# Optimization experiments

Measured on AMD Instinct MI355X. Metric: run time of the kernel, lower is better.

The kernel has to match this reference:

```python
import math
import jax, jax.numpy as jnp
import numpy as np

N = 100000       # nodes
K = 32           # fixed neighbor fanout
D_IN = 128
D_OUT = 128
TPERC = 0.45


def setup_inputs() -> dict:
    key = jax.random.key(0)
    k1, k2, k3 = jax.random.split(key, 3)
    x = jax.random.normal(k1, (N, D_IN), dtype=jnp.float32)
    # nn.Linear weight [out, in], no bias
    W = jax.random.normal(k2, (D_OUT, D_IN), dtype=jnp.float32) * (1.0 / math.sqrt(D_IN))
    nbrs = jax.random.randint(k3, (N, K), 0, N, dtype=jnp.int32)
    return {"x": x, "W": W, "nbrs": nbrs}


def reference(x, W, nbrs):
    # h = Linear(x): [N, D_OUT]
    h = jnp.einsum("nd,od->no", x, W)
    # gather neighbor messages: [N, K, D_OUT]
    msgs = h[nbrs]
    # per-channel sort over the neighbor axis (matches torch.sort(dim=0) per node)
    msgs = jnp.sort(msgs, axis=1)
    remove = math.floor(K * TPERC)  # static: 14
    if remove > 0:
        msgs = msgs[:, remove:K - remove]
    # trimmed mean over remaining neighbors; activation is identity (None)
    return jnp.mean(msgs, axis=1)
```

## Files before the change

kernel.cpp:

```cpp
#include <hip/hip_runtime.h>
#include <hip/hip_fp16.h>

#define NN 100000
#define KK 32
#define DD 128

typedef _Float16 v8h __attribute__((ext_vector_type(8)));
typedef _Float16 v4h __attribute__((ext_vector_type(4)));
typedef _Float16 v2h __attribute__((ext_vector_type(2)));
typedef float    v4f __attribute__((ext_vector_type(4)));

#define LDH 136

__global__ __launch_bounds__(256)
void gemm_mfma_kernel(const float* __restrict__ x, const float* __restrict__ W,
                      _Float16* __restrict__ h) {
    __shared__ _Float16 w_lds[DD * LDH];
    __shared__ _Float16 x_lds[128 * LDH];

    const int tid = threadIdx.x;
    const int block_row = blockIdx.x * 128;

    {
        const float4* ws = (const float4*)W;
        #pragma unroll
        for (int t = 0; t < 16; ++t) {
            const int fi = tid + 256 * t;
            const int r = fi >> 5, c4 = fi & 31;
            const float4 f = ws[fi];
            v4h p = { (_Float16)f.x, (_Float16)f.y, (_Float16)f.z, (_Float16)f.w };
            *(v4h*)&w_lds[r * LDH + c4 * 4] = p;
        }
    }
    {
        const float4* xs = (const float4*)x;
        #pragma unroll
        for (int t = 0; t < 16; ++t) {
            const int fi = tid + 256 * t;
            const int r = fi >> 5, c4 = fi & 31;
            const int gr = block_row + r;
            float4 f = make_float4(0.f, 0.f, 0.f, 0.f);
            if (gr < NN) f = xs[(size_t)gr * 32 + c4];
            v4h p = { (_Float16)f.x, (_Float16)f.y, (_Float16)f.z, (_Float16)f.w };
            *(v4h*)&x_lds[r * LDH + c4 * 4] = p;
        }
    }
    __syncthreads();

    const int wv   = tid >> 6;
    const int lane = tid & 63;
    const int m    = lane & 15;
    const int quad = lane >> 4;

    const v4f zero = {0.f, 0.f, 0.f, 0.f};
    v4f acc[2][8];
    #pragma unroll
    for (int nt = 0; nt < 2; ++nt)
        #pragma unroll
        for (int ot = 0; ot < 8; ++ot) acc[nt][ot] = zero;

    #pragma unroll
    for (int ks = 0; ks < 4; ++ks) {
        const int kb = ks * 32 + quad * 8;
        const v8h xf0 = *(const v8h*)&x_lds[(wv * 32 + m) * LDH + kb];
        const v8h xf1 = *(const v8h*)&x_lds[(wv * 32 + 16 + m) * LDH + kb];
        #pragma unroll
        for (int ot = 0; ot < 8; ++ot) {
            const v8h wf = *(const v8h*)&w_lds[(ot * 16 + m) * LDH + kb];
            acc[0][ot] = __builtin_amdgcn_mfma_f32_16x16x32_f16(wf, xf0, acc[0][ot], 0, 0, 0);
            acc[1][ot] = __builtin_amdgcn_mfma_f32_16x16x32_f16(wf, xf1, acc[1][ot], 0, 0, 0);
        }
    }

    #pragma unroll
    for (int nt = 0; nt < 2; ++nt) {
        const int xr = block_row + wv * 32 + nt * 16 + m;
        if (xr < NN) {
            #pragma unroll
            for (int ot = 0; ot < 8; ++ot) {
                const v4f a = acc[nt][ot];
                v4h p = { (_Float16)a.x, (_Float16)a.y, (_Float16)a.z, (_Float16)a.w };
                *(v4h*)&h[(size_t)xr * DD + ot * 16 + quad * 4] = p;
            }
        }
    }
}

#define CEA(i, l) do { const v2h lo_ = __builtin_elementwise_min(v[i], v[l]); \
                       const v2h hi_ = __builtin_elementwise_max(v[i], v[l]); \
                       v[i] = lo_; v[l] = hi_; } while (0)
#define CED(i, l) do { const v2h lo_ = __builtin_elementwise_min(v[i], v[l]); \
                       const v2h hi_ = __builtin_elementwise_max(v[i], v[l]); \
                       v[i] = hi_; v[l] = lo_; } while (0)

__global__ __launch_bounds__(256)
void trimmed_mean_kernel(const _Float16* __restrict__ h, const int* __restrict__ nbrs,
                         float* __restrict__ out) {
    __shared__ int s_nbr[4][KK];

    const int tid = threadIdx.x;
    const int row_base = blockIdx.x * 4;

    if (tid < 128)
        s_nbr[tid >> 5][tid & 31] = nbrs[(size_t)row_base * KK + tid];
    __syncthreads();

    const int c   = tid & 63;
    const int sub = tid >> 6;
    const int row = row_base + sub;

    const v2h* hb = (const v2h*)h;

    v2h v[KK];
    #pragma unroll
    for (int k = 0; k < KK; ++k) {
        const int idx = s_nbr[sub][k];
        v[k] = hb[(size_t)idx * 64 + c];
    }

    #pragma unroll
    for (int k = 2; k <= 16; k <<= 1) {
        #pragma unroll
        for (int j = k >> 1; j > 0; j >>= 1) {
            #pragma unroll
            for (int i = 0; i < KK; ++i) {
                const int l = i ^ j;
                if (l > i) {
                    if ((i & k) == 0) CEA(i, l);
                    else              CED(i, l);
                }
            }
        }
    }
    #pragma unroll
    for (int i = 0; i < 16; ++i) CEA(i, i + 16);
    #pragma unroll
    for (int i = 0; i < 8; ++i) { CEA(i, i + 8); CEA(i + 16, i + 24); }
    CEA(8, 12); CEA(9, 13); CEA(10, 14); CEA(11, 15);
    CEA(16, 20); CEA(17, 21); CEA(18, 22); CEA(19, 23);
    CEA(12, 14); CEA(13, 15); CEA(16, 18); CEA(17, 19);
    CEA(14, 15); CEA(16, 17);

    float2 o2;
    o2.x = ((float)v[14].x + (float)v[15].x + (float)v[16].x + (float)v[17].x) * 0.25f;
    o2.y = ((float)v[14].y + (float)v[15].y + (float)v[16].y + (float)v[17].y) * 0.25f;
    ((float2*)(out + (size_t)row * DD))[c] = o2;
}

extern "C" void kernel_launch(void* const* d_in, const int* in_sizes, int n_in,
                              void* d_out, int out_size, void* d_ws, size_t ws_size,
                              hipStream_t stream) {
    const float* x    = (const float*)d_in[0];
    const float* W    = (const float*)d_in[1];
    const int*   nbrs = (const int*)d_in[2];
    float*       out  = (float*)d_out;
    _Float16*    h    = (_Float16*)d_ws;

    (void)in_sizes; (void)n_in; (void)out_size; (void)ws_size;

    gemm_mfma_kernel<<<(NN + 127) / 128, 256, 0, stream>>>(x, W, h);
    trimmed_mean_kernel<<<NN / 4, 256, 0, stream>>>(h, nbrs, out);
}
```

Baseline: 230.3 us.

## Use odd-even merge sort network with 4 channels per thread in trimmed mean

Swaps the bitonic sorting network for Batcher odd-even merge sort on each 16-element half, generated at compile time. The second half is indexed in reverse so the bitonic merge can go straight to the middle elements. Each thread now loads 8 bytes (4 fp16 channels) per neighbor and handles 8 rows per block, which halves the gather instruction count and raises per-thread ILP. The cost is higher register pressure from 64 packed registers per thread, and the hand-written packed min/max inline asm may limit compiler scheduling.

```diff
diff --git a/kernel.cpp b/kernel.cpp
--- a/kernel.cpp
+++ b/kernel.cpp
@@ -86,65 +86,98 @@
     }
 }
 
-#define CEA(i, l) do { const v2h lo_ = __builtin_elementwise_min(v[i], v[l]); \
-                       const v2h hi_ = __builtin_elementwise_max(v[i], v[l]); \
-                       v[i] = lo_; v[l] = hi_; } while (0)
-#define CED(i, l) do { const v2h lo_ = __builtin_elementwise_min(v[i], v[l]); \
-                       const v2h hi_ = __builtin_elementwise_max(v[i], v[l]); \
-                       v[i] = hi_; v[l] = lo_; } while (0)
+struct CEp { signed char a, b; };
+struct Net16 { CEp ce[63]; };
+
+constexpr int oem_merge(CEp* out, int c, int lo, int n, int r) {
+    const int m = r * 2;
+    if (m < n) {
+        c = oem_merge(out, c, lo, n, m);
+        c = oem_merge(out, c, lo + r, n, m);
+        for (int i = lo + r; i + r < lo + n; i += m) {
+            out[c].a = (signed char)i; out[c].b = (signed char)(i + r); ++c;
+        }
+    } else {
+        out[c].a = (signed char)lo; out[c].b = (signed char)(lo + r); ++c;
+    }
+    return c;
+}
+constexpr int oem_sort(CEp* out, int c, int lo, int n) {
+    if (n > 1) {
+        const int m = n / 2;
+        c = oem_sort(out, c, lo, m);
+        c = oem_sort(out, c, lo + m, m);
+        c = oem_merge(out, c, lo, n, 1);
+    }
+    return c;
+}
+constexpr Net16 make_net16() {
+    Net16 net{};
+    (void)oem_sort(net.ce, 0, 0, 16);
+    return net;
+}
+constexpr Net16 NET16 = make_net16();
+
+constexpr int WMAP(int i) { return i < 16 ? i : 47 - i; }
+
+#define PKMIN(d, s0, s1) asm("v_pk_min_f16 %0, %1, %2" : "=v"(d) : "v"(s0), "v"(s1))
+#define PKMAX(d, s0, s1) asm("v_pk_max_f16 %0, %1, %2" : "=v"(d) : "v"(s0), "v"(s1))
+
+#define CEW(p, q) do {                                                  \
+    v2h na_, xa_, nb_, xb_;                                             \
+    PKMIN(na_, va[p], va[q]); PKMAX(xa_, va[p], va[q]);                 \
+    PKMIN(nb_, vb[p], vb[q]); PKMAX(xb_, vb[p], vb[q]);                 \
+    va[p] = na_; va[q] = xa_; vb[p] = nb_; vb[q] = xb_; } while (0)
 
 __global__ __launch_bounds__(256)
 void trimmed_mean_kernel(const _Float16* __restrict__ h, const int* __restrict__ nbrs,
                          float* __restrict__ out) {
-    __shared__ int s_nbr[4][KK];
+    __shared__ int s_nbr[8][KK];
 
     const int tid = threadIdx.x;
-    const int row_base = blockIdx.x * 4;
+    const int row_base = blockIdx.x * 8;
 
-    if (tid < 128)
-        s_nbr[tid >> 5][tid & 31] = nbrs[(size_t)row_base * KK + tid];
+    s_nbr[tid >> 5][tid & 31] = nbrs[(size_t)row_base * KK + tid];
     __syncthreads();
 
-    const int c   = tid & 63;
-    const int sub = tid >> 6;
-    const int row = row_base + sub;
+    const int brow = tid >> 5;
+    const int cq   = tid & 31;
+    const int row  = row_base + brow;
 
-    const v2h* hb = (const v2h*)h;
+    const uint2* hq = (const uint2*)h;
 
-    v2h v[KK];
+    v2h va[KK];
+    v2h vb[KK];
     #pragma unroll
     for (int k = 0; k < KK; ++k) {
-        const int idx = s_nbr[sub][k];
-        v[k] = hb[(size_t)idx * 64 + c];
+        const int idx = s_nbr[brow][k];
+        const uint2 u = hq[idx * 32 + cq];
+        va[k] = __builtin_bit_cast(v2h, u.x);
+        vb[k] = __builtin_bit_cast(v2h, u.y);
     }
 
     #pragma unroll
-    for (int k = 2; k <= 16; k <<= 1) {
-        #pragma unroll
-        for (int j = k >> 1; j > 0; j >>= 1) {
-            #pragma unroll
-            for (int i = 0; i < KK; ++i) {
-                const int l = i ^ j;
-                if (l > i) {
-                    if ((i & k) == 0) CEA(i, l);
-                    else              CED(i, l);
-                }
-            }
-        }
-    }
+    for (int t = 0; t < 63; ++t) CEW(NET16.ce[t].a, NET16.ce[t].b);
     #pragma unroll
-    for (int i = 0; i < 16; ++i) CEA(i, i + 16);
+    for (int t = 0; t < 63; ++t) CEW(NET16.ce[t].a + 16, NET16.ce[t].b + 16);
+
     #pragma unroll
-    for (int i = 0; i < 8; ++i) { CEA(i, i + 8); CEA(i + 16, i + 24); }
-    CEA(8, 12); CEA(9, 13); CEA(10, 14); CEA(11, 15);
-    CEA(16, 20); CEA(17, 21); CEA(18, 22); CEA(19, 23);
-    CEA(12, 14); CEA(13, 15); CEA(16, 18); CEA(17, 19);
-    CEA(14, 15); CEA(16, 17);
+    for (int i = 0; i < 16; ++i) CEW(WMAP(i), WMAP(i + 16));
+    #pragma unroll
+    for (int i = 0; i < 8; ++i) { CEW(WMAP(i), WMAP(i + 8));
+                                  CEW(WMAP(i + 16), WMAP(i + 24)); }
+    #pragma unroll
+    for (int i = 8; i < 12; ++i) { CEW(WMAP(i), WMAP(i + 4));
+                                   CEW(WMAP(i + 8), WMAP(i + 12)); }
+    CEW(WMAP(12), WMAP(14)); CEW(WMAP(13), WMAP(15));
+    CEW(WMAP(16), WMAP(18)); CEW(WMAP(17), WMAP(19));
 
-    float2 o2;
-    o2.x = ((float)v[14].x + (float)v[15].x + (float)v[16].x + (float)v[17].x) * 0.25f;
-    o2.y = ((float)v[14].y + (float)v[15].y + (float)v[16].y + (float)v[17].y) * 0.25f;
-    ((float2*)(out + (size_t)row * DD))[c] = o2;
+    float4 o;
+    o.x = ((float)va[14].x + (float)va[15].x + (float)va[31].x + (float)va[30].x) * 0.25f;
+    o.y = ((float)va[14].y + (float)va[15].y + (float)va[31].y + (float)va[30].y) * 0.25f;
+    o.z = ((float)vb[14].x + (float)vb[15].x + (float)vb[31].x + (float)vb[30].x) * 0.25f;
+    o.w = ((float)vb[14].y + (float)vb[15].y + (float)vb[31].y + (float)vb[30].y) * 0.25f;
+    ((float4*)(out + (size_t)row * DD))[cq] = o;
 }
 
 extern "C" void kernel_launch(void* const* d_in, const int* in_sizes, int n_in,
@@ -159,5 +192,5 @@
     (void)in_sizes; (void)n_in; (void)out_size; (void)ws_size;
 
     gemm_mfma_kernel<<<(NN + 127) / 128, 256, 0, stream>>>(x, W, h);
-    trimmed_mean_kernel<<<NN / 4, 256, 0, stream>>>(h, nbrs, out);
+    trimmed_mean_kernel<<<NN / 8, 256, 0, stream>>>(h, nbrs, out);
 }
```

Result: no change. 227.6 us (-1.2%).
